# Performance work log

Hardware: AMD Instinct MI355X
Metric: run time of the kernel (lower is better)

## Reference

```python
import jax, jax.numpy as jnp
import numpy as np

EPS_LN = 1e-5

def _ln(x, g, b):
    m = x.mean(-1, keepdims=True)
    v = jnp.var(x, axis=-1, keepdims=True)
    return (x - m) * jax.lax.rsqrt(v + EPS_LN) * g + b


def _forward(x, edge_attr, lin0_w, lin0_b, enn_w1, enn_b1, enn_g1, enn_b1n,
             enn_w2, enn_b2, enn_g2, enn_b2n, conv_bias,
             gru_w_ih, gru_w_hh, gru_b_ih, gru_b_hh,
             lstm_w_ih, lstm_w_hh, lstm_b_ih, lstm_b_hh,
             lin1_w, lin1_b, lin1_g, lin1_bn, lin2_w, lin2_b,
             edge_index, target_index, target_class):
    N = x.shape[0]
    D = lin0_w.shape[0]
    src, dst = edge_index[0], edge_index[1]

    out = jax.nn.relu(x @ lin0_w.T + lin0_b)            # [N, D]
    h = out                                             # GRU hidden state

    # edge NN -> per-edge weight matrix [E, D, D] (edge_attr constant across iters)
    e1 = jax.nn.relu(_ln(edge_attr @ enn_w1.T + enn_b1, enn_g1, enn_b1n))
    ew = _ln(e1 @ enn_w2.T + enn_b2, enn_g2, enn_b2n).reshape(-1, D, D)

    counts = jnp.clip(jax.ops.segment_sum(jnp.ones_like(dst, jnp.float32), dst, num_segments=N), 1.0)[:, None]

    for _ in range(3):
        msg = jnp.einsum('ed,edo->eo', out[src], ew)     # per-edge matmul
        agg = jax.ops.segment_sum(msg, dst, num_segments=N) / counts  # scatter-mean
        m = jax.nn.relu(agg + conv_bias)
        # GRU cell (seq len 1)
        gx = m @ gru_w_ih.T + gru_b_ih
        gh = h @ gru_w_hh.T + gru_b_hh
        xr, xz, xn = jnp.split(gx, 3, axis=-1)
        hr, hz, hn = jnp.split(gh, 3, axis=-1)
        r = jax.nn.sigmoid(xr + hr)
        z = jax.nn.sigmoid(xz + hz)
        n = jnp.tanh(xn + r * hn)
        h = (1.0 - z) * n + z * h
        out = h

    # Set2Set with batch_index = arange(N) (each node is its own set), 3 steps
    idx = jnp.arange(N)
    hl = jnp.zeros((N, D), x.dtype)
    cl = jnp.zeros((N, D), x.dtype)
    q_star = jnp.zeros((N, 2 * D), x.dtype)
    for _ in range(3):
        g = q_star @ lstm_w_ih.T + lstm_b_ih + hl @ lstm_w_hh.T + lstm_b_hh
        gi, gf, gg, go = jnp.split(g, 4, axis=-1)
        cl = jax.nn.sigmoid(gf) * cl + jax.nn.sigmoid(gi) * jnp.tanh(gg)
        hl = jax.nn.sigmoid(go) * jnp.tanh(cl)
        q = hl
        e = (out * q[idx]).sum(-1, keepdims=True)
        emax = jax.ops.segment_max(e, idx, num_segments=N)
        a = jnp.exp(e - emax[idx])
        a = a / (jax.ops.segment_sum(a, idx, num_segments=N)[idx] + 1e-16)
        r_pool = jax.ops.segment_sum(a * out, idx, num_segments=N)
        q_star = jnp.concatenate([q, r_pool], axis=-1)

    a0, a1 = target_index[0], target_index[1]
    cat = jnp.concatenate([out[a0], out[a1], q_star[a0], q_star[a1]], axis=-1)  # [P, 6D]
    p = jax.nn.relu(_ln(cat @ lin1_w.T + lin1_b, lin1_g, lin1_bn))
    p = p @ lin2_w.T + lin2_b                           # [P, 8]
    return jnp.take_along_axis(p, target_class[:, None], axis=1)[:, 0]


def setup_inputs() -> dict:
    N, E, P, F, D = 10000, 20000, 15000, 16, 64
    ks = iter(jax.random.split(jax.random.key(0), 40))
    def nrm(shape, s=0.1):
        return jax.random.normal(next(ks), shape, jnp.float32) * s
    return {
        'x': jax.random.normal(next(ks), (N, F), jnp.float32),
        'edge_attr': jax.random.normal(next(ks), (E, 4), jnp.float32),
        'lin0_w': nrm((D, F)), 'lin0_b': jnp.zeros((D,), jnp.float32),
        'enn_w1': nrm((128, 4)), 'enn_b1': jnp.zeros((128,), jnp.float32),
        'enn_g1': jnp.ones((128,), jnp.float32), 'enn_b1n': jnp.zeros((128,), jnp.float32),
        'enn_w2': nrm((D * D, 128), 0.05), 'enn_b2': jnp.zeros((D * D,), jnp.float32),
        'enn_g2': jnp.ones((D * D,), jnp.float32), 'enn_b2n': jnp.zeros((D * D,), jnp.float32),
        'conv_bias': jnp.zeros((D,), jnp.float32),
        'gru_w_ih': nrm((3 * D, D)), 'gru_w_hh': nrm((3 * D, D)),
        'gru_b_ih': jnp.zeros((3 * D,), jnp.float32), 'gru_b_hh': jnp.zeros((3 * D,), jnp.float32),
        'lstm_w_ih': nrm((4 * D, 2 * D)), 'lstm_w_hh': nrm((4 * D, D)),
        'lstm_b_ih': jnp.zeros((4 * D,), jnp.float32), 'lstm_b_hh': jnp.zeros((4 * D,), jnp.float32),
        'lin1_w': nrm((D, 6 * D)), 'lin1_b': jnp.zeros((D,), jnp.float32),
        'lin1_g': jnp.ones((D,), jnp.float32), 'lin1_bn': jnp.zeros((D,), jnp.float32),
        'lin2_w': nrm((8, D)), 'lin2_b': jnp.zeros((8,), jnp.float32),
        'edge_index': jax.random.randint(next(ks), (2, E), 0, N),
        'target_index': jax.random.randint(next(ks), (2, P), 0, N),
        'target_class': jax.random.randint(next(ks), (P,), 0, 8),
    }


def reference(x, edge_attr, lin0_w, lin0_b, enn_w1, enn_b1, enn_g1, enn_b1n,
              enn_w2, enn_b2, enn_g2, enn_b2n, conv_bias,
              gru_w_ih, gru_w_hh, gru_b_ih, gru_b_hh,
              lstm_w_ih, lstm_w_hh, lstm_b_ih, lstm_b_hh,
              lin1_w, lin1_b, lin1_g, lin1_bn, lin2_w, lin2_b,
              edge_index, target_index, target_class):
    return _forward(x, edge_attr, lin0_w, lin0_b, enn_w1, enn_b1, enn_g1, enn_b1n,
                    enn_w2, enn_b2, enn_g2, enn_b2n, conv_bias,
                    gru_w_ih, gru_w_hh, gru_b_ih, gru_b_hh,
                    lstm_w_ih, lstm_w_hh, lstm_b_ih, lstm_b_hh,
                    lin1_w, lin1_b, lin1_g, lin1_bn, lin2_w, lin2_b,
                    edge_index, target_index, target_class)
```

## Files before the change

### kernel.cpp

```cpp
#include <hip/hip_runtime.h>
#include <hip/hip_bf16.h>

#define EPS_LN 1e-5f

typedef __attribute__((ext_vector_type(8))) short bf16x8;
typedef __attribute__((ext_vector_type(4))) float f32x4;

__device__ __forceinline__ float dot4(float4 a, float4 b) {
    return a.x * b.x + a.y * b.y + a.z * b.z + a.w * b.w;
}
__device__ __forceinline__ float sigmoidf_(float x) { return 1.0f / (1.0f + expf(-x)); }

__device__ __forceinline__ float bfu2f(unsigned short u) {
    unsigned v = ((unsigned)u) << 16;
    float f;
    __builtin_memcpy(&f, &v, 4);
    return f;
}
__device__ __forceinline__ unsigned short f2bfu(float f) {
    __hip_bfloat16 h = __float2bfloat16(f);
    unsigned short u;
    __builtin_memcpy(&u, &h, 2);
    return u;
}
__device__ __forceinline__ unsigned pack2bf(float a, float b) {
    return (unsigned)f2bfu(a) | ((unsigned)f2bfu(b) << 16);
}

__global__ void lin0_kernel(const float* __restrict__ x, const float* __restrict__ w,
                            const float* __restrict__ b, float* __restrict__ h, int N) {
    int id = blockIdx.x * blockDim.x + threadIdx.x;
    if (id >= N * 64) return;
    int n = id >> 6, o = id & 63;
    const float* xr = x + n * 16;
    const float* wr = w + o * 16;
    float acc = b[o];
#pragma unroll
    for (int k = 0; k < 16; k++) acc += xr[k] * wr[k];
    h[id] = fmaxf(acc, 0.0f);
}

__global__ void count_kernel(const int* __restrict__ ei, float* __restrict__ counts, int E) {
    int e = blockIdx.x * blockDim.x + threadIdx.x;
    if (e < E) atomicAdd(&counts[ei[E + e]], 1.0f);
}

__global__ void w2prep_kernel(const float* __restrict__ w2, const float* __restrict__ g2,
                              const float* __restrict__ b2, unsigned short* __restrict__ w2g,
                              float* __restrict__ b2g, int n) {
    int id = blockIdx.x * blockDim.x + threadIdx.x;
    if (id < n) {
        int row = id >> 7;
        w2g[id] = f2bfu(w2[id] * g2[row]);
    }
    if (id < 4096) b2g[id] = b2[id] * g2[id];
}

__global__ __launch_bounds__(128) void edge_nn1_kernel(
    const float* __restrict__ ea, const float* __restrict__ w1, const float* __restrict__ b1,
    const float* __restrict__ g1, const float* __restrict__ b1n,
    unsigned short* __restrict__ e1h, unsigned short* __restrict__ e1l, int E) {
    int e = blockIdx.x, j = threadIdx.x;
    float a0 = ea[e * 4 + 0], a1 = ea[e * 4 + 1], a2 = ea[e * 4 + 2], a3 = ea[e * 4 + 3];
    const float* wr = w1 + j * 4;
    float z = b1[j] + a0 * wr[0] + a1 * wr[1] + a2 * wr[2] + a3 * wr[3];
    float s = z, s2 = z * z;
#pragma unroll
    for (int m = 32; m >= 1; m >>= 1) { s += __shfl_xor(s, m); s2 += __shfl_xor(s2, m); }
    __shared__ float ls[2], ls2[2];
    int wv = j >> 6;
    if ((j & 63) == 0) { ls[wv] = s; ls2[wv] = s2; }
    __syncthreads();
    float S = ls[0] + ls[1], S2 = ls2[0] + ls2[1];
    float mu = S * (1.0f / 128.0f);
    float var = fmaxf(S2 * (1.0f / 128.0f) - mu * mu, 0.0f);
    float inv = rsqrtf(var + EPS_LN);
    float v = fmaxf((z - mu) * inv * g1[j] + b1n[j], 0.0f);
    unsigned short hi = f2bfu(v);
    unsigned short lo = f2bfu(v - bfu2f(hi));
    e1h[e * 128 + j] = hi;
    e1l[e * 128 + j] = lo;
}

__global__ __launch_bounds__(128) void mpart_kernel(const float* __restrict__ w2,
                                                    const float* __restrict__ b2,
                                                    float* __restrict__ pMT, float* __restrict__ pv,
                                                    float* __restrict__ pcw, float* __restrict__ psb,
                                                    float* __restrict__ pc) {
    __shared__ float wL[16][128];
    __shared__ float b2L[16];
    int t = threadIdx.x, b = blockIdx.x;
#pragma unroll
    for (int i = 0; i < 16; i++) {
        int idx = t + i * 128;
        wL[idx >> 7][idx & 127] = w2[(size_t)(b * 16 + (idx >> 7)) * 128 + (idx & 127)];
    }
    if (t < 16) b2L[t] = b2[b * 16 + t];
    __syncthreads();
    int j = t;
    float wj[16];
#pragma unroll
    for (int o = 0; o < 16; o++) wj[o] = wL[o][j];
    float pvj = 0.f, pcwj = 0.f;
#pragma unroll
    for (int o = 0; o < 16; o++) { pvj += wj[o] * b2L[o]; pcwj += wj[o]; }
    for (int i4 = 0; i4 < 32; i4++) {
        float4 a = {0.f, 0.f, 0.f, 0.f};
#pragma unroll
        for (int o = 0; o < 16; o++) {
            float4 w4 = *(const float4*)&wL[o][i4 * 4];
            a.x += wj[o] * w4.x; a.y += wj[o] * w4.y;
            a.z += wj[o] * w4.z; a.w += wj[o] * w4.w;
        }
        *(float4*)&pMT[((size_t)b * 128 + j) * 128 + i4 * 4] = a;
    }
    pv[b * 128 + j] = pvj;
    pcw[b * 128 + j] = pcwj;
    if (t == 0) {
        float sb = 0.f, cc = 0.f;
#pragma unroll
        for (int o = 0; o < 16; o++) { sb += b2L[o]; cc += b2L[o] * b2L[o]; }
        psb[b] = sb;
        pc[b] = cc;
    }
}

__global__ __launch_bounds__(256) void mreduce_kernel(const float* __restrict__ pMT,
                                                      const float* __restrict__ pv,
                                                      const float* __restrict__ pcw,
                                                      const float* __restrict__ psb,
                                                      const float* __restrict__ pc,
                                                      unsigned short* __restrict__ mb,
                                                      float* __restrict__ varr,
                                                      float* __restrict__ cw,
                                                      float* __restrict__ sbc) {
    int fid = blockIdx.x * 256 + threadIdx.x;
    float s = 0.f;
    int j = fid >> 7, i = fid & 127;
    for (int b = 0; b < 256; b++) s += pMT[((size_t)b * 128 + j) * 128 + i];
    mb[fid] = f2bfu(s);
    if (fid < 128) {
        float sv = 0.f, sc = 0.f;
        for (int b = 0; b < 256; b++) { sv += pv[b * 128 + fid]; sc += pcw[b * 128 + fid]; }
        varr[fid] = sv;
        cw[fid] = sc;
    }
    if (fid == 0) {
        float sb = 0.f, cc = 0.f;
        for (int b = 0; b < 256; b++) { sb += psb[b]; cc += pc[b]; }
        sbc[0] = sb;
        sbc[1] = cc;
    }
}

__global__ __launch_bounds__(256) void stats_kernel(
    const unsigned short* __restrict__ e1h, const unsigned short* __restrict__ e1l,
    const unsigned short* __restrict__ mb, const float* __restrict__ cw,
    const float* __restrict__ varr, const float* __restrict__ sbc,
    float* __restrict__ stats, int E) {
    __shared__ __align__(16) unsigned char smem[65536];
    const int t = threadIdx.x;
    const int eb = blockIdx.x * 64;
#pragma unroll
    for (int r = 0; r < 4; r++) {
        int idx = t + r * 256;
        int row = idx >> 4, kseg = idx & 15;
        int er = eb + row;
        if (er >= E) er = E - 1;
        uint4 vh = *(const uint4*)&e1h[(size_t)er * 128 + kseg * 8];
        uint4 vl = *(const uint4*)&e1l[(size_t)er * 128 + kseg * 8];
        int off = row * 256 + ((kseg * 16) ^ ((row & 7) << 4));
        *(uint4*)(smem + off) = vh;
        *(uint4*)(smem + 16384 + off) = vl;
    }
#pragma unroll
    for (int r = 0; r < 8; r++) {
        int idx = t + r * 256;
        int row = idx >> 4, kseg = idx & 15;
        uint4 v = *(const uint4*)&mb[(size_t)row * 128 + kseg * 8];
        *(uint4*)(smem + 32768 + row * 256 + ((kseg * 16) ^ ((row & 7) << 4))) = v;
    }
    __syncthreads();
    const int w = t >> 6, lane = t & 63;
    const int wrow = w * 16;
    const int r16 = lane & 15, kg = lane >> 4;
    f32x4 tacc[8];
#pragma unroll
    for (int nj = 0; nj < 8; nj++) tacc[nj] = (f32x4){0.f, 0.f, 0.f, 0.f};
#pragma unroll
    for (int ks = 0; ks < 4; ks++) {
        int arow = wrow + r16;
        int koff = ks * 64 + kg * 16;
        bf16x8 ah = *(const bf16x8*)(smem + arow * 256 + (koff ^ ((arow & 7) << 4)));
        bf16x8 al = *(const bf16x8*)(smem + 16384 + arow * 256 + (koff ^ ((arow & 7) << 4)));
#pragma unroll
        for (int nj = 0; nj < 8; nj++) {
            int brow = nj * 16 + r16;
            bf16x8 bf = *(const bf16x8*)(smem + 32768 + brow * 256 + (koff ^ ((brow & 7) << 4)));
            tacc[nj] = __builtin_amdgcn_mfma_f32_16x16x32_bf16(ah, bf, tacc[nj], 0, 0, 0);
            tacc[nj] = __builtin_amdgcn_mfma_f32_16x16x32_bf16(al, bf, tacc[nj], 0, 0, 0);
        }
    }
    __syncthreads();
#pragma unroll
    for (int nj = 0; nj < 8; nj++)
#pragma unroll
        for (int r = 0; r < 4; r++) {
            int row = wrow + kg * 4 + r, col = nj * 16 + r16;
            *(float*)(smem + 32768 + row * 512 + col * 4) = tacc[nj][r];
        }
    __syncthreads();
    int el = t >> 2, q = t & 3;
    float s2p = 0.f, sp = 0.f, svp = 0.f;
    for (int kk = 0; kk < 32; kk++) {
        int k = q * 32 + kk;
        int boff = el * 256 + ((2 * k) ^ ((el & 7) << 4));
        float e1v = bfu2f(*(const unsigned short*)(smem + boff)) +
                    bfu2f(*(const unsigned short*)(smem + 16384 + boff));
        float tv = *(const float*)(smem + 32768 + el * 512 + k * 4);
        s2p += tv * e1v;
        sp += e1v * cw[k];
        svp += e1v * varr[k];
    }
    s2p += __shfl_xor(s2p, 1); s2p += __shfl_xor(s2p, 2);
    sp += __shfl_xor(sp, 1);   sp += __shfl_xor(sp, 2);
    svp += __shfl_xor(svp, 1); svp += __shfl_xor(svp, 2);
    if (q == 0) {
        int e = eb + el;
        if (e < E) {
            float S = sp + sbc[0];
            float S2 = s2p + 2.f * svp + sbc[1];
            float mu = S * (1.0f / 4096.0f);
            float var = fmaxf(S2 * (1.0f / 4096.0f) - mu * mu, 0.0f);
            float inv = rsqrtf(var + EPS_LN);
            stats[e * 2 + 0] = inv;
            stats[e * 2 + 1] = mu * inv;
        }
    }
}

__global__ __launch_bounds__(256) void zgemm_final(
    const unsigned short* __restrict__ e1h, const unsigned short* __restrict__ e1l,
    const unsigned short* __restrict__ w2g, const float* __restrict__ b2g,
    const float* __restrict__ g2, const float* __restrict__ b2n,
    const float* __restrict__ stats, unsigned short* __restrict__ zT, int E) {
    __shared__ __align__(16) unsigned char smem[65536];
    const int t = threadIdx.x;
    const int eb = blockIdx.x * 64;
    const int o0 = blockIdx.y * 2;
#pragma unroll
    for (int r = 0; r < 4; r++) {
        int idx = t + r * 256;
        int row = idx >> 4, kseg = idx & 15;
        int er = eb + row;
        if (er >= E) er = E - 1;
        uint4 vh = *(const uint4*)&e1h[(size_t)er * 128 + kseg * 8];
        uint4 vl = *(const uint4*)&e1l[(size_t)er * 128 + kseg * 8];
        int off = row * 256 + ((kseg * 16) ^ ((row & 7) << 4));
        *(uint4*)(smem + off) = vh;
        *(uint4*)(smem + 16384 + off) = vl;
    }
#pragma unroll
    for (int r = 0; r < 8; r++) {
        int idx = t + r * 256;
        int j = idx >> 4, kseg = idx & 15;
        int srcrow = ((j >> 1) << 6) + o0 + (j & 1);
        uint4 v = *(const uint4*)&w2g[(size_t)srcrow * 128 + kseg * 8];
        *(uint4*)(smem + 32768 + j * 256 + ((kseg * 16) ^ ((j & 7) << 4))) = v;
    }
    __syncthreads();
    const int w = t >> 6, lane = t & 63;
    const int wrow = (w >> 1) * 32, wcol = (w & 1) * 64;
    const int r16 = lane & 15, kg = lane >> 4;

    bf16x8 bfrag[4][4];
#pragma unroll
    for (int nj = 0; nj < 4; nj++)
#pragma unroll
        for (int ks = 0; ks < 4; ks++) {
            int row = wcol + nj * 16 + r16;
            int koff = ks * 64 + kg * 16;
            bfrag[nj][ks] = *(const bf16x8*)(smem + 32768 + row * 256 + (koff ^ ((row & 7) << 4)));
        }
    f32x4 acc[2][4];
#pragma unroll
    for (int mi = 0; mi < 2; mi++)
#pragma unroll
        for (int nj = 0; nj < 4; nj++) acc[mi][nj] = (f32x4){0.f, 0.f, 0.f, 0.f};
#pragma unroll
    for (int pass = 0; pass < 2; pass++) {
        int abase = pass * 16384;
#pragma unroll
        for (int ks = 0; ks < 4; ks++) {
            bf16x8 afrag[2];
#pragma unroll
            for (int mi = 0; mi < 2; mi++) {
                int row = wrow + mi * 16 + r16;
                int koff = ks * 64 + kg * 16;
                afrag[mi] = *(const bf16x8*)(smem + abase + row * 256 + (koff ^ ((row & 7) << 4)));
            }
#pragma unroll
            for (int mi = 0; mi < 2; mi++)
#pragma unroll
                for (int nj = 0; nj < 4; nj++)
                    acc[mi][nj] = __builtin_amdgcn_mfma_f32_16x16x32_bf16(
                        afrag[mi], bfrag[nj][ks], acc[mi][nj], 0, 0, 0);
        }
    }
    float bg[4], gg[4], bn[4];
#pragma unroll
    for (int nj = 0; nj < 4; nj++) {
        int j = wcol + nj * 16 + r16;
        int sj = ((j >> 1) << 6) + o0 + (j & 1);
        bg[nj] = b2g[sj];
        gg[nj] = g2[sj];
        bn[nj] = b2n[sj];
    }
    __syncthreads();
#pragma unroll
    for (int mi = 0; mi < 2; mi++)
#pragma unroll
        for (int r = 0; r < 4; r++) {
            int rowl = wrow + mi * 16 + kg * 4 + r;
            int eg = eb + rowl;
            if (eg >= E) eg = E - 1;
            float inv = stats[eg * 2 + 0], miv = stats[eg * 2 + 1];
#pragma unroll
            for (int nj = 0; nj < 4; nj++) {
                int j = wcol + nj * 16 + r16;
                float v = inv * (acc[mi][nj][r] + bg[nj]) - miv * gg[nj] + bn[nj];
                *(unsigned short*)(smem + rowl * 288 + ((j & 1) << 7) + ((j >> 1) << 1)) = f2bfu(v);
            }
        }
    __syncthreads();
#pragma unroll
    for (int r = 0; r < 4; r++) {
        int idx = t + r * 256;
        int row = idx >> 4, seg = idx & 15;
        if (eb + row < E) {
            uint4 v = *(const uint4*)(smem + row * 288 + seg * 16);
            *(uint4*)&zT[(size_t)(eb + row) * 4096 + (size_t)blockIdx.y * 128 + seg * 8] = v;
        }
    }
}

__global__ __launch_bounds__(256) void msg_kernel(const unsigned short* __restrict__ zT,
                                                  const float* __restrict__ h,
                                                  const int* __restrict__ ei,
                                                  float* __restrict__ agg, int E) {
    int t = threadIdx.x;
    int el = t >> 6, o = t & 63;
    int e = blockIdx.x * 4 + el;
    __shared__ float sL[4][64];
    int src = ei[e];
    int dstn = ei[E + e];
    sL[el][o] = h[src * 64 + o];
    __syncthreads();
    float acc = 0.f;
    const uint4* zp = (const uint4*)(zT + (size_t)e * 4096 + o * 64);
#pragma unroll
    for (int q = 0; q < 8; q++) {
        uint4 v = zp[q];
        const float* hp = &sL[el][q * 8];
        acc += __uint_as_float(v.x << 16) * hp[0] + __uint_as_float(v.x & 0xffff0000u) * hp[1];
        acc += __uint_as_float(v.y << 16) * hp[2] + __uint_as_float(v.y & 0xffff0000u) * hp[3];
        acc += __uint_as_float(v.z << 16) * hp[4] + __uint_as_float(v.z & 0xffff0000u) * hp[5];
        acc += __uint_as_float(v.w << 16) * hp[6] + __uint_as_float(v.w & 0xffff0000u) * hp[7];
    }
    atomicAdd(&agg[(size_t)dstn * 64 + o], acc);
}

__global__ __launch_bounds__(192) void gru_kernel(
    const float* __restrict__ agg, const float* __restrict__ counts, const float* __restrict__ cbias,
    const float* __restrict__ wih, const float* __restrict__ whh,
    const float* __restrict__ bih, const float* __restrict__ bhh, float* __restrict__ h, int N) {
    int t = threadIdx.x;
    int nb = blockIdx.x * 8;
    __shared__ __align__(16) float mL[8][64], hL[8][64], gxL[8][192], ghL[8][192];
    for (int idx = t; idx < 512; idx += 192) {
        int n = idx >> 6, k = idx & 63;
        int node = nb + n;
        float cnt = fmaxf(counts[node], 1.0f);
        mL[n][k] = fmaxf(agg[node * 64 + k] / cnt + cbias[k], 0.0f);
        hL[n][k] = h[node * 64 + k];
    }
    __syncthreads();
    {
        int j = t;
        float ax[8], ah[8];
#pragma unroll
        for (int n = 0; n < 8; n++) { ax[n] = 0.f; ah[n] = 0.f; }
        const float4* wi = (const float4*)(wih + j * 64);
        const float4* wh = (const float4*)(whh + j * 64);
#pragma unroll 4
        for (int k4 = 0; k4 < 16; k4++) {
            float4 wiv = wi[k4], whv = wh[k4];
#pragma unroll
            for (int n = 0; n < 8; n++) {
                ax[n] += dot4(wiv, *(const float4*)&mL[n][k4 * 4]);
                ah[n] += dot4(whv, *(const float4*)&hL[n][k4 * 4]);
            }
        }
        float bi = bih[j], bh = bhh[j];
#pragma unroll
        for (int n = 0; n < 8; n++) { gxL[n][j] = ax[n] + bi; ghL[n][j] = ah[n] + bh; }
    }
    __syncthreads();
    for (int idx = t; idx < 512; idx += 192) {
        int n = idx >> 6, k = idx & 63;
        int node = nb + n;
        float r = sigmoidf_(gxL[n][k] + ghL[n][k]);
        float zz = sigmoidf_(gxL[n][64 + k] + ghL[n][64 + k]);
        float nn = tanhf(gxL[n][128 + k] + r * ghL[n][128 + k]);
        h[node * 64 + k] = (1.0f - zz) * nn + zz * hL[n][k];
    }
}

__global__ void prep_wc_kernel(const float* __restrict__ wih, const float* __restrict__ whh,
                               const float* __restrict__ bih, const float* __restrict__ bhh,
                               float* __restrict__ wc, float* __restrict__ bsum) {
    int id = blockIdx.x * 256 + threadIdx.x;
    if (id < 16384) {
        int j = id >> 6, k = id & 63;
        wc[id] = wih[j * 128 + k] + whh[id];
    }
    if (id < 256) bsum[id] = bih[id] + bhh[id];
}

__global__ __launch_bounds__(256) void cout_kernel(const float* __restrict__ h,
                                                   const float* __restrict__ wih,
                                                   float* __restrict__ cout, int N) {
    int t = threadIdx.x, nb = blockIdx.x * 8;
    __shared__ __align__(16) float oL[8][64];
    for (int idx = t; idx < 512; idx += 256) {
        int n = idx >> 6, k = idx & 63;
        oL[n][k] = h[(nb + n) * 64 + k];
    }
    __syncthreads();
    int j = t;
    float acc[8];
#pragma unroll
    for (int n = 0; n < 8; n++) acc[n] = 0.f;
    const float* wr = wih + j * 128 + 64;
#pragma unroll 4
    for (int k4 = 0; k4 < 16; k4++) {
        float4 w4 = *(const float4*)&wr[k4 * 4];
#pragma unroll
        for (int n = 0; n < 8; n++) acc[n] += dot4(w4, *(const float4*)&oL[n][k4 * 4]);
    }
#pragma unroll
    for (int n = 0; n < 8; n++) cout[(size_t)(nb + n) * 256 + j] = acc[n];
}

__global__ void lstm_init_kernel(const float* __restrict__ bsum, float* __restrict__ hl,
                                 float* __restrict__ cl, int N) {
    int id = blockIdx.x * 256 + threadIdx.x;
    if (id >= N * 64) return;
    int j = id & 63;
    float gi = bsum[j], gg = bsum[128 + j], go = bsum[192 + j];
    float c = sigmoidf_(gi) * tanhf(gg);
    cl[id] = c;
    hl[id] = sigmoidf_(go) * tanhf(c);
}

__global__ __launch_bounds__(256) void lstm_step_kernel(const float* __restrict__ wc,
                                                        const float* __restrict__ bsum,
                                                        const float* __restrict__ cout,
                                                        float* __restrict__ hl,
                                                        float* __restrict__ cl, int N) {
    int t = threadIdx.x, nb = blockIdx.x * 8;
    __shared__ __align__(16) float hlL[8][64];
    __shared__ float gL[8][256];
    for (int idx = t; idx < 512; idx += 256) {
        int n = idx >> 6, k = idx & 63;
        hlL[n][k] = hl[(nb + n) * 64 + k];
    }
    __syncthreads();
    {
        int j = t;
        float acc[8];
#pragma unroll
        for (int n = 0; n < 8; n++) acc[n] = 0.f;
        const float4* w4p = (const float4*)(wc + j * 64);
#pragma unroll 4
        for (int k4 = 0; k4 < 16; k4++) {
            float4 w4 = w4p[k4];
#pragma unroll
            for (int n = 0; n < 8; n++) acc[n] += dot4(w4, *(const float4*)&hlL[n][k4 * 4]);
        }
        float bs = bsum[j];
#pragma unroll
        for (int n = 0; n < 8; n++) gL[n][j] = acc[n] + cout[(size_t)(nb + n) * 256 + j] + bs;
    }
    __syncthreads();
    for (int idx = t; idx < 512; idx += 256) {
        int n = idx >> 6, k = idx & 63;
        int node = nb + n;
        float gi = gL[n][k], gf = gL[n][64 + k], gg = gL[n][128 + k], go = gL[n][192 + k];
        float c = sigmoidf_(gf) * cl[node * 64 + k] + sigmoidf_(gi) * tanhf(gg);
        cl[node * 64 + k] = c;
        hl[node * 64 + k] = sigmoidf_(go) * tanhf(c);
    }
}

__global__ __launch_bounds__(256) void head_kernel(
    const float* __restrict__ h, const float* __restrict__ hl, const int* __restrict__ ti,
    const int* __restrict__ tc, const float* __restrict__ w1, const float* __restrict__ b1,
    const float* __restrict__ g1, const float* __restrict__ bn1, const float* __restrict__ w2,
    const float* __restrict__ b2, float* __restrict__ out, int P) {
    __shared__ uint2 w1q[6144];
    __shared__ float catL[4][384];
    int t = threadIdx.x;
    const float4* w1f4 = (const float4*)w1;
#pragma unroll
    for (int i = 0; i < 24; i++) {
        int f = t + i * 256;
        float4 v = w1f4[f];
        int j = f / 96, k4 = f - j * 96;
        w1q[k4 * 64 + j] = make_uint2(pack2bf(v.x, v.y), pack2bf(v.z, v.w));
    }
    int j = t & 63, pl = t >> 6;
    float b1j = b1[j], g1j = g1[j], bnj = bn1[j];
    __syncthreads();

    for (int pb = blockIdx.x * 4; pb < P; pb += gridDim.x * 4) {
#pragma unroll
        for (int i = 0; i < 6; i++) {
            int idx = t + i * 256;
            int p = idx / 384, kk = idx - p * 384;
            int pair = pb + p;
            if (pair >= P) pair = P - 1;
            int a0 = ti[pair], a1 = ti[P + pair];
            int s = kk >> 6, k = kk & 63;
            float v;
            if (s == 0 || s == 3) v = h[a0 * 64 + k];
            else if (s == 1 || s == 5) v = h[a1 * 64 + k];
            else if (s == 2) v = hl[a0 * 64 + k];
            else v = hl[a1 * 64 + k];
            catL[p][kk] = v;
        }
        __syncthreads();
        int pair = pb + pl;
        float acc = b1j;
#pragma unroll 8
        for (int k4 = 0; k4 < 96; k4++) {
            uint2 wv = w1q[k4 * 64 + j];
            float4 c = *(const float4*)&catL[pl][k4 * 4];
            acc += __uint_as_float(wv.x << 16) * c.x + __uint_as_float(wv.x & 0xffff0000u) * c.y;
            acc += __uint_as_float(wv.y << 16) * c.z + __uint_as_float(wv.y & 0xffff0000u) * c.w;
        }
        float s1 = acc, s2v = acc * acc;
#pragma unroll
        for (int m = 32; m >= 1; m >>= 1) { s1 += __shfl_xor(s1, m); s2v += __shfl_xor(s2v, m); }
        float mu = s1 * (1.0f / 64.0f);
        float var = fmaxf(s2v * (1.0f / 64.0f) - mu * mu, 0.0f);
        float p1 = fmaxf((acc - mu) * rsqrtf(var + EPS_LN) * g1j + bnj, 0.0f);
        int cls = tc[pair < P ? pair : P - 1];
        float part = p1 * w2[cls * 64 + j];
#pragma unroll
        for (int m = 32; m >= 1; m >>= 1) part += __shfl_xor(part, m);
        if (j == 0 && pair < P) out[pair] = part + b2[cls];
        __syncthreads();
    }
}

extern "C" void kernel_launch(void* const* d_in, const int* in_sizes, int n_in,
                              void* d_out, int out_size, void* d_ws, size_t ws_size,
                              hipStream_t stream) {
    const float* x = (const float*)d_in[0];
    const float* edge_attr = (const float*)d_in[1];
    const float* lin0_w = (const float*)d_in[2];
    const float* lin0_b = (const float*)d_in[3];
    const float* enn_w1 = (const float*)d_in[4];
    const float* enn_b1 = (const float*)d_in[5];
    const float* enn_g1 = (const float*)d_in[6];
    const float* enn_b1n = (const float*)d_in[7];
    const float* enn_w2 = (const float*)d_in[8];
    const float* enn_b2 = (const float*)d_in[9];
    const float* enn_g2 = (const float*)d_in[10];
    const float* enn_b2n = (const float*)d_in[11];
    const float* conv_bias = (const float*)d_in[12];
    const float* gru_w_ih = (const float*)d_in[13];
    const float* gru_w_hh = (const float*)d_in[14];
    const float* gru_b_ih = (const float*)d_in[15];
    const float* gru_b_hh = (const float*)d_in[16];
    const float* lstm_w_ih = (const float*)d_in[17];
    const float* lstm_w_hh = (const float*)d_in[18];
    const float* lstm_b_ih = (const float*)d_in[19];
    const float* lstm_b_hh = (const float*)d_in[20];
    const float* lin1_w = (const float*)d_in[21];
    const float* lin1_b = (const float*)d_in[22];
    const float* lin1_g = (const float*)d_in[23];
    const float* lin1_bn = (const float*)d_in[24];
    const float* lin2_w = (const float*)d_in[25];
    const float* lin2_b = (const float*)d_in[26];
    const int* edge_index = (const int*)d_in[27];
    const int* target_index = (const int*)d_in[28];
    const int* target_class = (const int*)d_in[29];

    const int N = in_sizes[0] / 16;
    const int E = in_sizes[27] / 2;
    const int P = in_sizes[29];

    size_t off = 0;
    auto carve = [&](size_t bytes) {
        void* p = (char*)d_ws + off;
        off += (bytes + 255) & ~(size_t)255;
        return p;
    };
    unsigned short* zbuf = (unsigned short*)carve((size_t)E * 4096 * 2);
    unsigned short* e1h = (unsigned short*)carve((size_t)E * 128 * 2);
    unsigned short* e1l = (unsigned short*)carve((size_t)E * 128 * 2);
    unsigned short* w2g = (unsigned short*)carve((size_t)4096 * 128 * 2);
    float* b2g = (float*)carve((size_t)4096 * 4);
    float* hbuf = (float*)carve((size_t)N * 64 * 4);
    float* agg = (float*)carve((size_t)N * 64 * 4);
    float* counts = (float*)carve((size_t)N * 4);
    float* hl = (float*)carve((size_t)N * 64 * 4);
    float* cl = (float*)carve((size_t)N * 64 * 4);
    float* cout_b = (float*)carve((size_t)N * 256 * 4);
    float* wc = (float*)carve((size_t)256 * 64 * 4);
    float* bsum = (float*)carve((size_t)256 * 4);
    float* stats = (float*)carve((size_t)E * 2 * 4);
    unsigned short* mb = (unsigned short*)carve((size_t)128 * 128 * 2);
    float* varr = (float*)carve((size_t)128 * 4);
    float* cw = (float*)carve((size_t)128 * 4);
    float* sbc = (float*)carve((size_t)2 * 4);
    float* pv = (float*)carve((size_t)256 * 128 * 4);
    float* pcw = (float*)carve((size_t)256 * 128 * 4);
    float* psb = (float*)carve((size_t)256 * 4);
    float* pc = (float*)carve((size_t)256 * 4);
    float* pMT = (float*)zbuf;
    (void)ws_size;

    hipMemsetAsync(counts, 0, (size_t)N * 4, stream);
    lin0_kernel<<<(N * 64 + 255) / 256, 256, 0, stream>>>(x, lin0_w, lin0_b, hbuf, N);
    count_kernel<<<(E + 255) / 256, 256, 0, stream>>>(edge_index, counts, E);
    edge_nn1_kernel<<<E, 128, 0, stream>>>(edge_attr, enn_w1, enn_b1, enn_g1, enn_b1n, e1h, e1l, E);
    w2prep_kernel<<<(4096 * 128 + 255) / 256, 256, 0, stream>>>(enn_w2, enn_g2, enn_b2, w2g, b2g,
                                                                4096 * 128);
    mpart_kernel<<<256, 128, 0, stream>>>(enn_w2, enn_b2, pMT, pv, pcw, psb, pc);
    mreduce_kernel<<<64, 256, 0, stream>>>(pMT, pv, pcw, psb, pc, mb, varr, cw, sbc);
    stats_kernel<<<(E + 63) / 64, 256, 0, stream>>>(e1h, e1l, mb, cw, varr, sbc, stats, E);
    {
        dim3 g((E + 63) / 64, 32);
        zgemm_final<<<g, 256, 0, stream>>>(e1h, e1l, w2g, b2g, enn_g2, enn_b2n, stats, zbuf, E);
    }

    for (int it = 0; it < 3; it++) {
        hipMemsetAsync(agg, 0, (size_t)N * 64 * 4, stream);
        msg_kernel<<<E / 4, 256, 0, stream>>>(zbuf, hbuf, edge_index, agg, E);
        gru_kernel<<<N / 8, 192, 0, stream>>>(agg, counts, conv_bias, gru_w_ih, gru_w_hh,
                                              gru_b_ih, gru_b_hh, hbuf, N);
    }

    prep_wc_kernel<<<64, 256, 0, stream>>>(lstm_w_ih, lstm_w_hh, lstm_b_ih, lstm_b_hh, wc, bsum);
    cout_kernel<<<N / 8, 256, 0, stream>>>(hbuf, lstm_w_ih, cout_b, N);
    lstm_init_kernel<<<(N * 64 + 255) / 256, 256, 0, stream>>>(bsum, hl, cl, N);
    lstm_step_kernel<<<N / 8, 256, 0, stream>>>(wc, bsum, cout_b, hl, cl, N);
    lstm_step_kernel<<<N / 8, 256, 0, stream>>>(wc, bsum, cout_b, hl, cl, N);

    head_kernel<<<512, 256, 0, stream>>>(hbuf, hl, target_index, target_class, lin1_w, lin1_b,
                                         lin1_g, lin1_bn, lin2_w, lin2_b, (float*)d_out, P);
}
```

Measured before the change: 457.6 us.

## Fuse edge-weight GEMM into message kernel instead of materializing per-edge matrices

Removes the precomputed per-edge bf16 DxD weight tensor and its large write and three rereads. Each iteration now recomputes the edge-NN second-layer GEMM with MFMA inside the message kernel and contracts it with the source hidden state on the fly. The LayerNorm affine terms are folded algebraically into per-node corrections (h·g, h·b, h·bn) from a small new kernel. This trades memory traffic for three times the GEMM compute. It also drops the low-part (e1l) bf16 term, so precision drops, and it adds more atomics.

```diff
diff --git a/kernel.cpp b/kernel.cpp
--- a/kernel.cpp
+++ b/kernel.cpp
@@ -239,135 +239,158 @@
     }
 }
 
-__global__ __launch_bounds__(256) void zgemm_final(
-    const unsigned short* __restrict__ e1h, const unsigned short* __restrict__ e1l,
-    const unsigned short* __restrict__ w2g, const float* __restrict__ b2g,
-    const float* __restrict__ g2, const float* __restrict__ b2n,
-    const float* __restrict__ stats, unsigned short* __restrict__ zT, int E) {
-    __shared__ __align__(16) unsigned char smem[65536];
+__global__ __launch_bounds__(192) void corr_kernel(const float* __restrict__ h,
+                                                   const float* __restrict__ g2,
+                                                   const float* __restrict__ b2g,
+                                                   const float* __restrict__ b2n,
+                                                   float* __restrict__ hG, float* __restrict__ hB,
+                                                   float* __restrict__ hN, int N) {
+    __shared__ float wL[3][64][64];
+    __shared__ float hh[8][64];
+    int t = threadIdx.x, nb = blockIdx.x * 8;
+    for (int idx = t; idx < 12288; idx += 192) {
+        int mat = idx >> 12, rem = idx & 4095;
+        ((float*)wL)[idx] = mat == 0 ? g2[rem] : (mat == 1 ? b2g[rem] : b2n[rem]);
+    }
+    for (int idx = t; idx < 512; idx += 192)
+        hh[idx >> 6][idx & 63] = h[(size_t)(nb + (idx >> 6)) * 64 + (idx & 63)];
+    __syncthreads();
+    int mat = t >> 6, j = t & 63;
+    float* outp = mat == 0 ? hG : (mat == 1 ? hB : hN);
+#pragma unroll
+    for (int n = 0; n < 8; n++) {
+        float a = 0.f;
+#pragma unroll 8
+        for (int d = 0; d < 64; d++) a += hh[n][d] * wL[mat][d][j];
+        outp[(size_t)(nb + n) * 64 + j] = a;
+    }
+}
+
+__global__ __launch_bounds__(512) void msg_fused(
+    const unsigned short* __restrict__ e1h, const unsigned short* __restrict__ w2g,
+    const float* __restrict__ h, const float* __restrict__ stats,
+    const float* __restrict__ hG, const float* __restrict__ hB, const float* __restrict__ hN,
+    const int* __restrict__ ei, float* __restrict__ agg, int E) {
+    __shared__ __align__(16) unsigned char BsB[32768];
+    __shared__ float hL[128][68];
+    __shared__ int srcL[128], dstL[128];
+    __shared__ float invL[128], mivL[128];
     const int t = threadIdx.x;
-    const int eb = blockIdx.x * 64;
-    const int o0 = blockIdx.y * 2;
-#pragma unroll
-    for (int r = 0; r < 4; r++) {
-        int idx = t + r * 256;
-        int row = idx >> 4, kseg = idx & 15;
-        int er = eb + row;
+    const int eb = blockIdx.x * 128;
+    const int y = blockIdx.y;
+
+    if (t < 128) {
+        int e = eb + t;
+        if (e >= E) e = E - 1;
+        srcL[t] = ei[e];
+        dstL[t] = ei[E + e];
+        invL[t] = stats[e * 2 + 0];
+        mivL[t] = stats[e * 2 + 1];
+    }
+    __syncthreads();
+    {
+        int e_loc = t >> 2, part = t & 3;
+        const float4* hp = (const float4*)(h + (size_t)srcL[e_loc] * 64 + part * 16);
+        float4* dp = (float4*)&hL[e_loc][part * 16];
+        dp[0] = hp[0]; dp[1] = hp[1]; dp[2] = hp[2]; dp[3] = hp[3];
+    }
+
+    const int w = t >> 6, lane = t & 63;
+    const int wave_e = w >> 1, wave_c = w & 1;
+    const int r16 = lane & 15, kg = lane >> 4;
+
+    bf16x8 afrag[2][4];
+#pragma unroll
+    for (int mi = 0; mi < 2; mi++) {
+        int er = eb + wave_e * 32 + mi * 16 + r16;
         if (er >= E) er = E - 1;
-        uint4 vh = *(const uint4*)&e1h[(size_t)er * 128 + kseg * 8];
-        uint4 vl = *(const uint4*)&e1l[(size_t)er * 128 + kseg * 8];
-        int off = row * 256 + ((kseg * 16) ^ ((row & 7) << 4));
-        *(uint4*)(smem + off) = vh;
-        *(uint4*)(smem + 16384 + off) = vl;
-    }
-#pragma unroll
-    for (int r = 0; r < 8; r++) {
-        int idx = t + r * 256;
-        int j = idx >> 4, kseg = idx & 15;
-        int srcrow = ((j >> 1) << 6) + o0 + (j & 1);
-        uint4 v = *(const uint4*)&w2g[(size_t)srcrow * 128 + kseg * 8];
-        *(uint4*)(smem + 32768 + j * 256 + ((kseg * 16) ^ ((j & 7) << 4))) = v;
-    }
-    __syncthreads();
-    const int w = t >> 6, lane = t & 63;
-    const int wrow = (w >> 1) * 32, wcol = (w & 1) * 64;
-    const int r16 = lane & 15, kg = lane >> 4;
-
-    bf16x8 bfrag[4][4];
-#pragma unroll
-    for (int nj = 0; nj < 4; nj++)
+        const char* ab = (const char*)e1h + (size_t)er * 256;
+#pragma unroll
+        for (int ks = 0; ks < 4; ks++) afrag[mi][ks] = *(const bf16x8*)(ab + ks * 64 + kg * 16);
+    }
+
+    f32x4 msg_acc[2][4];
+#pragma unroll
+    for (int mi = 0; mi < 2; mi++)
+#pragma unroll
+        for (int nj = 0; nj < 4; nj++) msg_acc[mi][nj] = (f32x4){0.f, 0.f, 0.f, 0.f};
+
+    const char* wybase = (const char*)w2g + (size_t)y * 2048 * 256;
+    uint4 vv[4];
+#pragma unroll
+    for (int q = 0; q < 4; q++) {
+        int s = q * 512 + t;
+        int row = s >> 4, xs = s & 15;
+        vv[q] = *(const uint4*)(wybase + row * 256 + ((xs * 16) ^ ((row & 7) << 4)));
+    }
+
+    for (int ch = 0; ch < 16; ch++) {
+#pragma unroll
+        for (int q = 0; q < 4; q++) *(uint4*)(BsB + (q * 512 + t) * 16) = vv[q];
+        __syncthreads();
+        if (ch + 1 < 16) {
+            const char* cb = wybase + (size_t)(ch + 1) * 32768;
+#pragma unroll
+            for (int q = 0; q < 4; q++) {
+                int s = q * 512 + t;
+                int row = s >> 4, xs = s & 15;
+                vv[q] = *(const uint4*)(cb + row * 256 + ((xs * 16) ^ ((row & 7) << 4)));
+            }
+        }
+        f32x4 acc[2][4];
+#pragma unroll
+        for (int mi = 0; mi < 2; mi++)
+#pragma unroll
+            for (int nj = 0; nj < 4; nj++) acc[mi][nj] = (f32x4){0.f, 0.f, 0.f, 0.f};
 #pragma unroll
         for (int ks = 0; ks < 4; ks++) {
-            int row = wcol + nj * 16 + r16;
-            int koff = ks * 64 + kg * 16;
-            bfrag[nj][ks] = *(const bf16x8*)(smem + 32768 + row * 256 + (koff ^ ((row & 7) << 4)));
-        }
-    f32x4 acc[2][4];
-#pragma unroll
-    for (int mi = 0; mi < 2; mi++)
-#pragma unroll
-        for (int nj = 0; nj < 4; nj++) acc[mi][nj] = (f32x4){0.f, 0.f, 0.f, 0.f};
-#pragma unroll
-    for (int pass = 0; pass < 2; pass++) {
-        int abase = pass * 16384;
-#pragma unroll
-        for (int ks = 0; ks < 4; ks++) {
-            bf16x8 afrag[2];
-#pragma unroll
-            for (int mi = 0; mi < 2; mi++) {
-                int row = wrow + mi * 16 + r16;
+            bf16x8 bfr[4];
+#pragma unroll
+            for (int nj = 0; nj < 4; nj++) {
+                int j = wave_c * 64 + nj * 16 + r16;
                 int koff = ks * 64 + kg * 16;
-                afrag[mi] = *(const bf16x8*)(smem + abase + row * 256 + (koff ^ ((row & 7) << 4)));
+                bfr[nj] = *(const bf16x8*)(BsB + j * 256 + (koff ^ ((j & 7) << 4)));
             }
 #pragma unroll
             for (int mi = 0; mi < 2; mi++)
 #pragma unroll
                 for (int nj = 0; nj < 4; nj++)
                     acc[mi][nj] = __builtin_amdgcn_mfma_f32_16x16x32_bf16(
-                        afrag[mi], bfrag[nj][ks], acc[mi][nj], 0, 0, 0);
-        }
-    }
-    float bg[4], gg[4], bn[4];
-#pragma unroll
-    for (int nj = 0; nj < 4; nj++) {
-        int j = wcol + nj * 16 + r16;
-        int sj = ((j >> 1) << 6) + o0 + (j & 1);
-        bg[nj] = b2g[sj];
-        gg[nj] = g2[sj];
-        bn[nj] = b2n[sj];
-    }
-    __syncthreads();
+                        afrag[mi][ks], bfr[nj], acc[mi][nj], 0, 0, 0);
+        }
+        int d = y * 32 + ch * 2 + wave_c;
+#pragma unroll
+        for (int mi = 0; mi < 2; mi++)
+#pragma unroll
+            for (int r = 0; r < 4; r++) {
+                int e_loc = wave_e * 32 + mi * 16 + kg * 4 + r;
+                float hv = hL[e_loc][d];
+#pragma unroll
+                for (int nj = 0; nj < 4; nj++) msg_acc[mi][nj][r] += hv * acc[mi][nj][r];
+            }
+        __syncthreads();
+    }
+
 #pragma unroll
     for (int mi = 0; mi < 2; mi++)
 #pragma unroll
         for (int r = 0; r < 4; r++) {
-            int rowl = wrow + mi * 16 + kg * 4 + r;
-            int eg = eb + rowl;
-            if (eg >= E) eg = E - 1;
-            float inv = stats[eg * 2 + 0], miv = stats[eg * 2 + 1];
-#pragma unroll
-            for (int nj = 0; nj < 4; nj++) {
-                int j = wcol + nj * 16 + r16;
-                float v = inv * (acc[mi][nj][r] + bg[nj]) - miv * gg[nj] + bn[nj];
-                *(unsigned short*)(smem + rowl * 288 + ((j & 1) << 7) + ((j >> 1) << 1)) = f2bfu(v);
+            int e_loc = wave_e * 32 + mi * 16 + kg * 4 + r;
+            int e = eb + e_loc;
+            if (e < E) {
+                float inv = invL[e_loc], miv = mivL[e_loc];
+                int sn = srcL[e_loc], dn = dstL[e_loc];
+#pragma unroll
+                for (int nj = 0; nj < 4; nj++) {
+                    int o = nj * 16 + r16;
+                    float val = inv * msg_acc[mi][nj][r];
+                    if (y == 0 && wave_c == 0)
+                        val += inv * hB[(size_t)sn * 64 + o] - miv * hG[(size_t)sn * 64 + o] +
+                               hN[(size_t)sn * 64 + o];
+                    atomicAdd(&agg[(size_t)dn * 64 + o], val);
+                }
             }
         }
-    __syncthreads();
-#pragma unroll
-    for (int r = 0; r < 4; r++) {
-        int idx = t + r * 256;
-        int row = idx >> 4, seg = idx & 15;
-        if (eb + row < E) {
-            uint4 v = *(const uint4*)(smem + row * 288 + seg * 16);
-            *(uint4*)&zT[(size_t)(eb + row) * 4096 + (size_t)blockIdx.y * 128 + seg * 8] = v;
-        }
-    }
-}
-
-__global__ __launch_bounds__(256) void msg_kernel(const unsigned short* __restrict__ zT,
-                                                  const float* __restrict__ h,
-                                                  const int* __restrict__ ei,
-                                                  float* __restrict__ agg, int E) {
-    int t = threadIdx.x;
-    int el = t >> 6, o = t & 63;
-    int e = blockIdx.x * 4 + el;
-    __shared__ float sL[4][64];
-    int src = ei[e];
-    int dstn = ei[E + e];
-    sL[el][o] = h[src * 64 + o];
-    __syncthreads();
-    float acc = 0.f;
-    const uint4* zp = (const uint4*)(zT + (size_t)e * 4096 + o * 64);
-#pragma unroll
-    for (int q = 0; q < 8; q++) {
-        uint4 v = zp[q];
-        const float* hp = &sL[el][q * 8];
-        acc += __uint_as_float(v.x << 16) * hp[0] + __uint_as_float(v.x & 0xffff0000u) * hp[1];
-        acc += __uint_as_float(v.y << 16) * hp[2] + __uint_as_float(v.y & 0xffff0000u) * hp[3];
-        acc += __uint_as_float(v.z << 16) * hp[4] + __uint_as_float(v.z & 0xffff0000u) * hp[5];
-        acc += __uint_as_float(v.w << 16) * hp[6] + __uint_as_float(v.w & 0xffff0000u) * hp[7];
-    }
-    atomicAdd(&agg[(size_t)dstn * 64 + o], acc);
 }
 
 __global__ __launch_bounds__(192) void gru_kernel(
@@ -608,7 +631,6 @@
         off += (bytes + 255) & ~(size_t)255;
         return p;
     };
-    unsigned short* zbuf = (unsigned short*)carve((size_t)E * 4096 * 2);
     unsigned short* e1h = (unsigned short*)carve((size_t)E * 128 * 2);
     unsigned short* e1l = (unsigned short*)carve((size_t)E * 128 * 2);
     unsigned short* w2g = (unsigned short*)carve((size_t)4096 * 128 * 2);
@@ -630,7 +652,10 @@
     float* pcw = (float*)carve((size_t)256 * 128 * 4);
     float* psb = (float*)carve((size_t)256 * 4);
     float* pc = (float*)carve((size_t)256 * 4);
-    float* pMT = (float*)zbuf;
+    float* hG = (float*)carve((size_t)N * 64 * 4);
+    float* hB = (float*)carve((size_t)N * 64 * 4);
+    float* hN = (float*)carve((size_t)N * 64 * 4);
+    float* pMT = (float*)carve((size_t)256 * 128 * 128 * 4);
     (void)ws_size;
 
     hipMemsetAsync(counts, 0, (size_t)N * 4, stream);
@@ -642,14 +667,14 @@
     mpart_kernel<<<256, 128, 0, stream>>>(enn_w2, enn_b2, pMT, pv, pcw, psb, pc);
     mreduce_kernel<<<64, 256, 0, stream>>>(pMT, pv, pcw, psb, pc, mb, varr, cw, sbc);
     stats_kernel<<<(E + 63) / 64, 256, 0, stream>>>(e1h, e1l, mb, cw, varr, sbc, stats, E);
-    {
-        dim3 g((E + 63) / 64, 32);
-        zgemm_final<<<g, 256, 0, stream>>>(e1h, e1l, w2g, b2g, enn_g2, enn_b2n, stats, zbuf, E);
-    }
 
     for (int it = 0; it < 3; it++) {
+        corr_kernel<<<N / 8, 192, 0, stream>>>(hbuf, enn_g2, b2g, enn_b2n, hG, hB, hN, N);
         hipMemsetAsync(agg, 0, (size_t)N * 64 * 4, stream);
-        msg_kernel<<<E / 4, 256, 0, stream>>>(zbuf, hbuf, edge_index, agg, E);
+        {
+            dim3 g((E + 127) / 128, 2);
+            msg_fused<<<g, 512, 0, stream>>>(e1h, w2g, hbuf, stats, hG, hB, hN, edge_index, agg, E);
+        }
         gru_kernel<<<N / 8, 192, 0, stream>>>(agg, counts, conv_bias, gru_w_ih, gru_w_hh,
                                               gru_b_ih, gru_b_hh, hbuf, N);
     }
```

Result: slower. 597.5 us (+30.6%).

## Fuse small prep kernels, merge memsets, and remap zgemm grid to column-major order

Applied to the files above, without the earlier changes.

Merges lin0 and the edge-count pass into one init kernel, folds the w2 bf16 prep into mpart, and folds the LSTM weight/bias prep and initial state into the cout kernel, cutting several launches. The three per-iteration agg memsets become a single upfront memset over three separate agg buffers. The zgemm grid is transposed so column tiles vary fastest and each tile covers contiguous output columns, which simplifies the store layout. pMT gets its own workspace region instead of aliasing zbuf, which enlarges the workspace footprint.

```diff
diff --git a/kernel.cpp b/kernel.cpp
--- a/kernel.cpp
+++ b/kernel.cpp
@@ -27,33 +27,21 @@
     return (unsigned)f2bfu(a) | ((unsigned)f2bfu(b) << 16);
 }
 
-__global__ void lin0_kernel(const float* __restrict__ x, const float* __restrict__ w,
-                            const float* __restrict__ b, float* __restrict__ h, int N) {
+__global__ void init_kernel(const float* __restrict__ x, const float* __restrict__ w,
+                            const float* __restrict__ b, float* __restrict__ h,
+                            const int* __restrict__ ei, float* __restrict__ counts,
+                            int N, int E) {
     int id = blockIdx.x * blockDim.x + threadIdx.x;
-    if (id >= N * 64) return;
-    int n = id >> 6, o = id & 63;
-    const float* xr = x + n * 16;
-    const float* wr = w + o * 16;
-    float acc = b[o];
-#pragma unroll
-    for (int k = 0; k < 16; k++) acc += xr[k] * wr[k];
-    h[id] = fmaxf(acc, 0.0f);
-}
-
-__global__ void count_kernel(const int* __restrict__ ei, float* __restrict__ counts, int E) {
-    int e = blockIdx.x * blockDim.x + threadIdx.x;
-    if (e < E) atomicAdd(&counts[ei[E + e]], 1.0f);
-}
-
-__global__ void w2prep_kernel(const float* __restrict__ w2, const float* __restrict__ g2,
-                              const float* __restrict__ b2, unsigned short* __restrict__ w2g,
-                              float* __restrict__ b2g, int n) {
-    int id = blockIdx.x * blockDim.x + threadIdx.x;
-    if (id < n) {
-        int row = id >> 7;
-        w2g[id] = f2bfu(w2[id] * g2[row]);
-    }
-    if (id < 4096) b2g[id] = b2[id] * g2[id];
+    if (id < N * 64) {
+        int n = id >> 6, o = id & 63;
+        const float* xr = x + n * 16;
+        const float* wr = w + o * 16;
+        float acc = b[o];
+#pragma unroll
+        for (int k = 0; k < 16; k++) acc += xr[k] * wr[k];
+        h[id] = fmaxf(acc, 0.0f);
+    }
+    if (id < E) atomicAdd(&counts[ei[E + id]], 1.0f);
 }
 
 __global__ __launch_bounds__(128) void edge_nn1_kernel(
@@ -84,6 +72,9 @@
 
 __global__ __launch_bounds__(128) void mpart_kernel(const float* __restrict__ w2,
                                                     const float* __restrict__ b2,
+                                                    const float* __restrict__ g2,
+                                                    unsigned short* __restrict__ w2g,
+                                                    float* __restrict__ b2g,
                                                     float* __restrict__ pMT, float* __restrict__ pv,
                                                     float* __restrict__ pcw, float* __restrict__ psb,
                                                     float* __restrict__ pc) {
@@ -97,6 +88,12 @@
     }
     if (t < 16) b2L[t] = b2[b * 16 + t];
     __syncthreads();
+#pragma unroll
+    for (int o = 0; o < 16; o++) {
+        int row = b * 16 + o;
+        w2g[(size_t)row * 128 + t] = f2bfu(wL[o][t] * g2[row]);
+    }
+    if (t < 16) b2g[b * 16 + t] = b2L[t] * g2[b * 16 + t];
     int j = t;
     float wj[16];
 #pragma unroll
@@ -246,8 +243,9 @@
     const float* __restrict__ stats, unsigned short* __restrict__ zT, int E) {
     __shared__ __align__(16) unsigned char smem[65536];
     const int t = threadIdx.x;
-    const int eb = blockIdx.x * 64;
-    const int o0 = blockIdx.y * 2;
+    const int eb = blockIdx.y * 64;
+    const int cb = blockIdx.x * 128;
+    const int o0 = blockIdx.x * 2;
 #pragma unroll
     for (int r = 0; r < 4; r++) {
         int idx = t + r * 256;
@@ -264,7 +262,7 @@
     for (int r = 0; r < 8; r++) {
         int idx = t + r * 256;
         int j = idx >> 4, kseg = idx & 15;
-        int srcrow = ((j >> 1) << 6) + o0 + (j & 1);
+        int srcrow = ((j & 63) << 6) + o0 + (j >> 6);
         uint4 v = *(const uint4*)&w2g[(size_t)srcrow * 128 + kseg * 8];
         *(uint4*)(smem + 32768 + j * 256 + ((kseg * 16) ^ ((j & 7) << 4))) = v;
     }
@@ -311,7 +309,7 @@
 #pragma unroll
     for (int nj = 0; nj < 4; nj++) {
         int j = wcol + nj * 16 + r16;
-        int sj = ((j >> 1) << 6) + o0 + (j & 1);
+        int sj = ((j & 63) << 6) + o0 + (j >> 6);
         bg[nj] = b2g[sj];
         gg[nj] = g2[sj];
         bn[nj] = b2n[sj];
@@ -329,7 +327,7 @@
             for (int nj = 0; nj < 4; nj++) {
                 int j = wcol + nj * 16 + r16;
                 float v = inv * (acc[mi][nj][r] + bg[nj]) - miv * gg[nj] + bn[nj];
-                *(unsigned short*)(smem + rowl * 288 + ((j & 1) << 7) + ((j >> 1) << 1)) = f2bfu(v);
+                *(unsigned short*)(smem + rowl * 272 + j * 2) = f2bfu(v);
             }
         }
     __syncthreads();
@@ -338,8 +336,8 @@
         int idx = t + r * 256;
         int row = idx >> 4, seg = idx & 15;
         if (eb + row < E) {
-            uint4 v = *(const uint4*)(smem + row * 288 + seg * 16);
-            *(uint4*)&zT[(size_t)(eb + row) * 4096 + (size_t)blockIdx.y * 128 + seg * 8] = v;
+            uint4 v = *(const uint4*)(smem + row * 272 + seg * 16);
+            *(uint4*)&zT[(size_t)(eb + row) * 4096 + cb + seg * 8] = v;
         }
     }
 }
@@ -416,20 +414,11 @@
     }
 }
 
-__global__ void prep_wc_kernel(const float* __restrict__ wih, const float* __restrict__ whh,
-                               const float* __restrict__ bih, const float* __restrict__ bhh,
-                               float* __restrict__ wc, float* __restrict__ bsum) {
-    int id = blockIdx.x * 256 + threadIdx.x;
-    if (id < 16384) {
-        int j = id >> 6, k = id & 63;
-        wc[id] = wih[j * 128 + k] + whh[id];
-    }
-    if (id < 256) bsum[id] = bih[id] + bhh[id];
-}
-
-__global__ __launch_bounds__(256) void cout_kernel(const float* __restrict__ h,
-                                                   const float* __restrict__ wih,
-                                                   float* __restrict__ cout, int N) {
+__global__ __launch_bounds__(256) void coutprep_kernel(
+    const float* __restrict__ h, const float* __restrict__ wih, const float* __restrict__ whh,
+    const float* __restrict__ bih, const float* __restrict__ bhh,
+    float* __restrict__ cout, float* __restrict__ wc,
+    float* __restrict__ hl, float* __restrict__ cl, int N) {
     int t = threadIdx.x, nb = blockIdx.x * 8;
     __shared__ __align__(16) float oL[8][64];
     for (int idx = t; idx < 512; idx += 256) {
@@ -437,34 +426,42 @@
         oL[n][k] = h[(nb + n) * 64 + k];
     }
     __syncthreads();
-    int j = t;
-    float acc[8];
-#pragma unroll
-    for (int n = 0; n < 8; n++) acc[n] = 0.f;
-    const float* wr = wih + j * 128 + 64;
+    {
+        float acc[8];
+#pragma unroll
+        for (int n = 0; n < 8; n++) acc[n] = 0.f;
+        const float* wr = wih + t * 128 + 64;
 #pragma unroll 4
-    for (int k4 = 0; k4 < 16; k4++) {
-        float4 w4 = *(const float4*)&wr[k4 * 4];
-#pragma unroll
-        for (int n = 0; n < 8; n++) acc[n] += dot4(w4, *(const float4*)&oL[n][k4 * 4]);
-    }
-#pragma unroll
-    for (int n = 0; n < 8; n++) cout[(size_t)(nb + n) * 256 + j] = acc[n];
-}
-
-__global__ void lstm_init_kernel(const float* __restrict__ bsum, float* __restrict__ hl,
-                                 float* __restrict__ cl, int N) {
-    int id = blockIdx.x * 256 + threadIdx.x;
-    if (id >= N * 64) return;
-    int j = id & 63;
-    float gi = bsum[j], gg = bsum[128 + j], go = bsum[192 + j];
-    float c = sigmoidf_(gi) * tanhf(gg);
-    cl[id] = c;
-    hl[id] = sigmoidf_(go) * tanhf(c);
+        for (int k4 = 0; k4 < 16; k4++) {
+            float4 w4 = *(const float4*)&wr[k4 * 4];
+#pragma unroll
+            for (int n = 0; n < 8; n++) acc[n] += dot4(w4, *(const float4*)&oL[n][k4 * 4]);
+        }
+#pragma unroll
+        for (int n = 0; n < 8; n++) cout[(size_t)(nb + n) * 256 + t] = acc[n];
+    }
+    if (blockIdx.x < 64) {
+        int id = blockIdx.x * 256 + t;
+        int j = id >> 6, k = id & 63;
+        wc[id] = wih[j * 128 + k] + whh[id];
+    }
+    if (t < 64) {
+        float gi = bih[t] + bhh[t];
+        float gg = bih[128 + t] + bhh[128 + t];
+        float go = bih[192 + t] + bhh[192 + t];
+        float c0 = sigmoidf_(gi) * tanhf(gg);
+        float h0 = sigmoidf_(go) * tanhf(c0);
+#pragma unroll
+        for (int n = 0; n < 8; n++) {
+            cl[(nb + n) * 64 + t] = c0;
+            hl[(nb + n) * 64 + t] = h0;
+        }
+    }
 }
 
 __global__ __launch_bounds__(256) void lstm_step_kernel(const float* __restrict__ wc,
-                                                        const float* __restrict__ bsum,
+                                                        const float* __restrict__ bih,
+                                                        const float* __restrict__ bhh,
                                                         const float* __restrict__ cout,
                                                         float* __restrict__ hl,
                                                         float* __restrict__ cl, int N) {
@@ -477,20 +474,19 @@
     }
     __syncthreads();
     {
-        int j = t;
         float acc[8];
 #pragma unroll
         for (int n = 0; n < 8; n++) acc[n] = 0.f;
-        const float4* w4p = (const float4*)(wc + j * 64);
+        const float4* w4p = (const float4*)(wc + t * 64);
 #pragma unroll 4
         for (int k4 = 0; k4 < 16; k4++) {
             float4 w4 = w4p[k4];
 #pragma unroll
             for (int n = 0; n < 8; n++) acc[n] += dot4(w4, *(const float4*)&hlL[n][k4 * 4]);
         }
-        float bs = bsum[j];
-#pragma unroll
-        for (int n = 0; n < 8; n++) gL[n][j] = acc[n] + cout[(size_t)(nb + n) * 256 + j] + bs;
+        float bs = bih[t] + bhh[t];
+#pragma unroll
+        for (int n = 0; n < 8; n++) gL[n][t] = acc[n] + cout[(size_t)(nb + n) * 256 + t] + bs;
     }
     __syncthreads();
     for (int idx = t; idx < 512; idx += 256) {
@@ -614,13 +610,14 @@
     unsigned short* w2g = (unsigned short*)carve((size_t)4096 * 128 * 2);
     float* b2g = (float*)carve((size_t)4096 * 4);
     float* hbuf = (float*)carve((size_t)N * 64 * 4);
-    float* agg = (float*)carve((size_t)N * 64 * 4);
-    float* counts = (float*)carve((size_t)N * 4);
+    float* counts = (float*)carve((size_t)N * 4 + (size_t)3 * N * 64 * 4);
+    float* agg0 = counts + N;
+    float* agg1 = agg0 + (size_t)N * 64;
+    float* agg2 = agg1 + (size_t)N * 64;
     float* hl = (float*)carve((size_t)N * 64 * 4);
     float* cl = (float*)carve((size_t)N * 64 * 4);
     float* cout_b = (float*)carve((size_t)N * 256 * 4);
     float* wc = (float*)carve((size_t)256 * 64 * 4);
-    float* bsum = (float*)carve((size_t)256 * 4);
     float* stats = (float*)carve((size_t)E * 2 * 4);
     unsigned short* mb = (unsigned short*)carve((size_t)128 * 128 * 2);
     float* varr = (float*)carve((size_t)128 * 4);
@@ -630,35 +627,32 @@
     float* pcw = (float*)carve((size_t)256 * 128 * 4);
     float* psb = (float*)carve((size_t)256 * 4);
     float* pc = (float*)carve((size_t)256 * 4);
-    float* pMT = (float*)zbuf;
+    float* pMT = (float*)carve((size_t)256 * 128 * 128 * 4);
     (void)ws_size;
 
-    hipMemsetAsync(counts, 0, (size_t)N * 4, stream);
-    lin0_kernel<<<(N * 64 + 255) / 256, 256, 0, stream>>>(x, lin0_w, lin0_b, hbuf, N);
-    count_kernel<<<(E + 255) / 256, 256, 0, stream>>>(edge_index, counts, E);
+    hipMemsetAsync(counts, 0, (size_t)N * 4 + (size_t)3 * N * 64 * 4, stream);
+    init_kernel<<<(N * 64 + 255) / 256, 256, 0, stream>>>(x, lin0_w, lin0_b, hbuf, edge_index,
+                                                          counts, N, E);
     edge_nn1_kernel<<<E, 128, 0, stream>>>(edge_attr, enn_w1, enn_b1, enn_g1, enn_b1n, e1h, e1l, E);
-    w2prep_kernel<<<(4096 * 128 + 255) / 256, 256, 0, stream>>>(enn_w2, enn_g2, enn_b2, w2g, b2g,
-                                                                4096 * 128);
-    mpart_kernel<<<256, 128, 0, stream>>>(enn_w2, enn_b2, pMT, pv, pcw, psb, pc);
+    mpart_kernel<<<256, 128, 0, stream>>>(enn_w2, enn_b2, enn_g2, w2g, b2g, pMT, pv, pcw, psb, pc);
     mreduce_kernel<<<64, 256, 0, stream>>>(pMT, pv, pcw, psb, pc, mb, varr, cw, sbc);
     stats_kernel<<<(E + 63) / 64, 256, 0, stream>>>(e1h, e1l, mb, cw, varr, sbc, stats, E);
     {
-        dim3 g((E + 63) / 64, 32);
+        dim3 g(32, (E + 63) / 64);
         zgemm_final<<<g, 256, 0, stream>>>(e1h, e1l, w2g, b2g, enn_g2, enn_b2n, stats, zbuf, E);
     }
 
+    float* aggs[3] = {agg0, agg1, agg2};
     for (int it = 0; it < 3; it++) {
-        hipMemsetAsync(agg, 0, (size_t)N * 64 * 4, stream);
-        msg_kernel<<<E / 4, 256, 0, stream>>>(zbuf, hbuf, edge_index, agg, E);
-        gru_kernel<<<N / 8, 192, 0, stream>>>(agg, counts, conv_bias, gru_w_ih, gru_w_hh,
+        msg_kernel<<<E / 4, 256, 0, stream>>>(zbuf, hbuf, edge_index, aggs[it], E);
+        gru_kernel<<<N / 8, 192, 0, stream>>>(aggs[it], counts, conv_bias, gru_w_ih, gru_w_hh,
                                               gru_b_ih, gru_b_hh, hbuf, N);
     }
 
-    prep_wc_kernel<<<64, 256, 0, stream>>>(lstm_w_ih, lstm_w_hh, lstm_b_ih, lstm_b_hh, wc, bsum);
-    cout_kernel<<<N / 8, 256, 0, stream>>>(hbuf, lstm_w_ih, cout_b, N);
-    lstm_init_kernel<<<(N * 64 + 255) / 256, 256, 0, stream>>>(bsum, hl, cl, N);
-    lstm_step_kernel<<<N / 8, 256, 0, stream>>>(wc, bsum, cout_b, hl, cl, N);
-    lstm_step_kernel<<<N / 8, 256, 0, stream>>>(wc, bsum, cout_b, hl, cl, N);
+    coutprep_kernel<<<N / 8, 256, 0, stream>>>(hbuf, lstm_w_ih, lstm_w_hh, lstm_b_ih, lstm_b_hh,
+                                               cout_b, wc, hl, cl, N);
+    lstm_step_kernel<<<N / 8, 256, 0, stream>>>(wc, lstm_b_ih, lstm_b_hh, cout_b, hl, cl, N);
+    lstm_step_kernel<<<N / 8, 256, 0, stream>>>(wc, lstm_b_ih, lstm_b_hh, cout_b, hl, cl, N);
 
     head_kernel<<<512, 256, 0, stream>>>(hbuf, hl, target_index, target_class, lin1_w, lin1_b,
                                          lin1_g, lin1_bn, lin2_w, lin2_b, (float*)d_out, P);
```

Result: faster. 432.7 us (-5.4%).
